# Kernel optimization log

Hardware: AMD Instinct MI355X
Metric: run time of the kernel (lower is better)

## Reference

```python
import jax, jax.numpy as jnp
import numpy as np

LATENT = 64
COND = 768
HEADS = 8
R = 8           # LoRA rank
SCALING = 1.0   # lora_alpha / r
SCALE = (LATENT / HEADS) ** -0.5


def _lora_linear(x, W, b, A, B):
    # loralib-style: y = x W^T + b + scaling * (x A^T) B^T
    return x @ W.T + b + SCALING * ((x @ A.T) @ B.T)


def setup_inputs() -> dict:
    key = jax.random.key(0)
    ks = jax.random.split(key, 20)
    B, C, H, W_ = 16, LATENT, 64, 64
    L = 77
    z = jax.random.normal(ks[0], (B, C, H, W_), dtype=jnp.float32)
    cond = jax.random.normal(ks[1], (B, L, COND), dtype=jnp.float32)

    def lin(k, out_d, in_d):
        k1, k2, k3 = jax.random.split(k, 3)
        W = jax.random.normal(k1, (out_d, in_d), dtype=jnp.float32) * 0.02
        b = jnp.zeros((out_d,), dtype=jnp.float32)
        A = jax.random.normal(k2, (R, in_d), dtype=jnp.float32) * 0.02
        Bm = jax.random.normal(k3, (out_d, R), dtype=jnp.float32) * 0.02
        return W, b, A, Bm

    Wq, bq, Aq, Bq = lin(ks[2], LATENT, LATENT)
    Wk, bk, Ak, Bk = lin(ks[3], LATENT, COND)
    Wv, bv, Av, Bv = lin(ks[4], LATENT, COND)
    Wo, bo, Ao, Bo = lin(ks[5], LATENT, LATENT)
    return dict(z=z, cond=cond,
                Wq=Wq, bq=bq, Aq=Aq, Bq=Bq,
                Wk=Wk, bk=bk, Ak=Ak, Bk=Bk,
                Wv=Wv, bv=bv, Av=Av, Bv=Bv,
                Wo=Wo, bo=bo, Ao=Ao, Bo=Bo)


def reference(z, cond, Wq, bq, Aq, Bq, Wk, bk, Ak, Bk, Wv, bv, Av, Bv, Wo, bo, Ao, Bo):
    B, C, H, W_ = z.shape
    hw = H * W_
    dh = C // HEADS
    z_flat = z.transpose(0, 2, 3, 1).reshape(B, hw, C)  # [B, hw, C]

    q = _lora_linear(z_flat, Wq, bq, Aq, Bq)   # [B, hw, C]
    k = _lora_linear(cond, Wk, bk, Ak, Bk)     # [B, L, C]
    v = _lora_linear(cond, Wv, bv, Av, Bv)     # [B, L, C]

    q = q.reshape(B, hw, HEADS, dh).transpose(0, 2, 1, 3)  # [B, h, hw, dh]
    k = k.reshape(B, -1, HEADS, dh).transpose(0, 2, 1, 3)  # [B, h, L, dh]
    v = v.reshape(B, -1, HEADS, dh).transpose(0, 2, 1, 3)

    dots = jnp.einsum('bhqd,bhkd->bhqk', q, k) * SCALE  # [B, h, hw, L]
    attn = jax.nn.softmax(dots, axis=-1)
    out = jnp.einsum('bhqk,bhkd->bhqd', attn, v)        # [B, h, hw, dh]
    out = out.transpose(0, 2, 1, 3).reshape(B, hw, C)
    out = _lora_linear(out, Wo, bo, Ao, Bo)
    return out.reshape(B, H, W_, C).transpose(0, 3, 1, 2)  # [B, C, H, W]
```

## Files before the change

kernel.cpp:

```cpp
#include <hip/hip_runtime.h>


#define HW   4096
#define CHN  64
#define LSEQ 77
#define CD   768
#define NB   16

#define OFF_WQ 0
#define OFF_WK 4096
#define OFF_WV 53248
#define OFF_WO 102400
#define OFF_K  106496
#define OFF_V  185344

#define QF 0.51011784563163f

__global__ __launch_bounds__(256) void prep_weights(
    const float* __restrict__ Wq, const float* __restrict__ Aq, const float* __restrict__ Bq,
    const float* __restrict__ Wk, const float* __restrict__ Ak, const float* __restrict__ Bk,
    const float* __restrict__ Wv, const float* __restrict__ Av, const float* __restrict__ Bv,
    const float* __restrict__ Wo, const float* __restrict__ Ao, const float* __restrict__ Bo,
    float* __restrict__ ws) {
  int idx = blockIdx.x * 256 + threadIdx.x;
  const float *W, *A, *Bm;
  float* out;
  int in_d, local;
  float scale = 1.0f;
  if (idx < 4096)        { W = Wq; A = Aq; Bm = Bq; out = ws + OFF_WQ; in_d = 64;  local = idx; scale = QF; }
  else if (idx < 53248)  { W = Wk; A = Ak; Bm = Bk; out = ws + OFF_WK; in_d = 768; local = idx - 4096; }
  else if (idx < 102400) { W = Wv; A = Av; Bm = Bv; out = ws + OFF_WV; in_d = 768; local = idx - 53248; }
  else                   { W = Wo; A = Ao; Bm = Bo; out = ws + OFF_WO; in_d = 64;  local = idx - 102400; }
  int co = local & 63;
  int c  = local >> 6;
  float val = W[co * in_d + c];
  #pragma unroll
  for (int r = 0; r < 8; r++) val += Bm[co * 8 + r] * A[r * in_d + c];
  out[local] = val * scale;
}

__global__ __launch_bounds__(256) void kvproj5(
    const float* __restrict__ cond,
    const float* __restrict__ wkT,
    const float* __restrict__ wvT,
    const float* __restrict__ bk, const float* __restrict__ bv,
    float* __restrict__ kbuf,
    float* __restrict__ vbuf) {
  __shared__ float xs[4 * CD];
  __shared__ float red[16 * 256];
  int kv = blockIdx.y;
  int r0 = blockIdx.x * 4;
  int t  = threadIdx.x;
  int l  = t & 63;
  int q  = __builtin_amdgcn_readfirstlane(t >> 6);
  int l16 = l & 15;
  int cs  = l >> 4;

  {
    const float4* src = (const float4*)(cond + r0 * CD);
    float4* dst = (float4*)xs;
    #pragma unroll
    for (int i = 0; i < 3; i++) dst[t + 256 * i] = src[t + 256 * i];
  }
  __syncthreads();

  const float4* wT4 = (const float4*)(kv ? wvT : wkT);
  float4 a0 = make_float4(0.f, 0.f, 0.f, 0.f);
  float4 a1 = a0, a2 = a0, a3 = a0;
  int cbase = q * 192 + cs;
  #pragma unroll 8
  for (int it = 0; it < 48; it++) {
    int c = cbase + 4 * it;
    float4 w  = wT4[c * 16 + l16];
    float x0 = xs[0 * CD + c];
    float x1 = xs[1 * CD + c];
    float x2 = xs[2 * CD + c];
    float x3 = xs[3 * CD + c];
    a0.x = fmaf(x0, w.x, a0.x); a0.y = fmaf(x0, w.y, a0.y);
    a0.z = fmaf(x0, w.z, a0.z); a0.w = fmaf(x0, w.w, a0.w);
    a1.x = fmaf(x1, w.x, a1.x); a1.y = fmaf(x1, w.y, a1.y);
    a1.z = fmaf(x1, w.z, a1.z); a1.w = fmaf(x1, w.w, a1.w);
    a2.x = fmaf(x2, w.x, a2.x); a2.y = fmaf(x2, w.y, a2.y);
    a2.z = fmaf(x2, w.z, a2.z); a2.w = fmaf(x2, w.w, a2.w);
    a3.x = fmaf(x3, w.x, a3.x); a3.y = fmaf(x3, w.y, a3.y);
    a3.z = fmaf(x3, w.z, a3.z); a3.w = fmaf(x3, w.w, a3.w);
  }

  {
    float4* redq = (float4*)(red + (q * 4 + cs) * 256);
    redq[0 * 16 + l16] = a0;
    redq[1 * 16 + l16] = a1;
    redq[2 * 16 + l16] = a2;
    redq[3 * 16 + l16] = a3;
  }
  __syncthreads();

  int r  = t >> 6;
  int co = t & 63;
  float val = (kv ? bv : bk)[co];
  #pragma unroll
  for (int g = 0; g < 16; g++) val += red[g * 256 + r * 64 + co];
  (kv ? vbuf : kbuf)[(r0 + r) * 64 + co] = val;
}

__global__ __launch_bounds__(256, 2) void megattn(
    const float* __restrict__ z,
    const float* __restrict__ wqT,
    const float* __restrict__ bq,
    const float* __restrict__ kbuf,
    const float* __restrict__ vbuf,
    const float* __restrict__ woT,
    const float* __restrict__ bo,
    float* __restrict__ out) {
  __shared__ float smem[LSEQ * 64 * 2];
  int b  = blockIdx.y;
  int p0 = blockIdx.x * 128;
  int t  = threadIdx.x;
  int h  = t >> 5;
  int pl = t & 31;

  float* ks = smem;
  float* vs = smem + LSEQ * 64;
  {
    const float4* ksrc = (const float4*)(kbuf + b * LSEQ * 64);
    const float4* vsrc = (const float4*)(vbuf + b * LSEQ * 64);
    float4* kd = (float4*)ks;
    float4* vd = (float4*)vs;
    for (int i = t; i < LSEQ * 16; i += 256) { kd[i] = ksrc[i]; vd[i] = vsrc[i]; }
  }

  float qr[4][8];
  {
    const float4 b0 = *(const float4*)(bq + 8 * h);
    const float4 b1 = *(const float4*)(bq + 8 * h + 4);
    #pragma unroll
    for (int i = 0; i < 4; i++) {
      qr[i][0] = b0.x * QF; qr[i][1] = b0.y * QF; qr[i][2] = b0.z * QF; qr[i][3] = b0.w * QF;
      qr[i][4] = b1.x * QF; qr[i][5] = b1.y * QF; qr[i][6] = b1.z * QF; qr[i][7] = b1.w * QF;
    }
  }
  const float* zb = z + b * (CHN * HW) + p0 + pl;
  #pragma unroll 4
  for (int c = 0; c < 64; c++) {
    float4 w0 = *(const float4*)(wqT + c * 64 + 8 * h);
    float4 w1 = *(const float4*)(wqT + c * 64 + 8 * h + 4);
    float zv[4];
    #pragma unroll
    for (int i = 0; i < 4; i++) zv[i] = zb[c * HW + 32 * i];
    #pragma unroll
    for (int i = 0; i < 4; i++) {
      qr[i][0] = fmaf(zv[i], w0.x, qr[i][0]);
      qr[i][1] = fmaf(zv[i], w0.y, qr[i][1]);
      qr[i][2] = fmaf(zv[i], w0.z, qr[i][2]);
      qr[i][3] = fmaf(zv[i], w0.w, qr[i][3]);
      qr[i][4] = fmaf(zv[i], w1.x, qr[i][4]);
      qr[i][5] = fmaf(zv[i], w1.y, qr[i][5]);
      qr[i][6] = fmaf(zv[i], w1.z, qr[i][6]);
      qr[i][7] = fmaf(zv[i], w1.w, qr[i][7]);
    }
  }
  __syncthreads();

  float acc[4][8];
  float li[4];
  #pragma unroll
  for (int i = 0; i < 4; i++) {
    li[i] = 0.f;
    #pragma unroll
    for (int d = 0; d < 8; d++) acc[i][d] = 0.f;
  }
  #pragma unroll 2
  for (int j = 0; j < LSEQ; j++) {
    float4 k0 = *(const float4*)(ks + j * 64 + 8 * h);
    float4 k1 = *(const float4*)(ks + j * 64 + 8 * h + 4);
    float4 v0 = *(const float4*)(vs + j * 64 + 8 * h);
    float4 v1 = *(const float4*)(vs + j * 64 + 8 * h + 4);
    #pragma unroll
    for (int i = 0; i < 4; i++) {
      float s = qr[i][0] * k0.x;
      s = fmaf(qr[i][1], k0.y, s);
      s = fmaf(qr[i][2], k0.z, s);
      s = fmaf(qr[i][3], k0.w, s);
      s = fmaf(qr[i][4], k1.x, s);
      s = fmaf(qr[i][5], k1.y, s);
      s = fmaf(qr[i][6], k1.z, s);
      s = fmaf(qr[i][7], k1.w, s);
      float e = __builtin_amdgcn_exp2f(s);
      li[i] += e;
      acc[i][0] = fmaf(e, v0.x, acc[i][0]);
      acc[i][1] = fmaf(e, v0.y, acc[i][1]);
      acc[i][2] = fmaf(e, v0.z, acc[i][2]);
      acc[i][3] = fmaf(e, v0.w, acc[i][3]);
      acc[i][4] = fmaf(e, v1.x, acc[i][4]);
      acc[i][5] = fmaf(e, v1.y, acc[i][5]);
      acc[i][6] = fmaf(e, v1.z, acc[i][6]);
      acc[i][7] = fmaf(e, v1.w, acc[i][7]);
    }
  }
  __syncthreads();

  float* ao = smem;
  #pragma unroll
  for (int i = 0; i < 4; i++) {
    float inv = 1.0f / li[i];
    int p = pl + 32 * i;
    #pragma unroll
    for (int d = 0; d < 8; d++) ao[p * 65 + 8 * h + d] = acc[i][d] * inv;
  }
  __syncthreads();

  int q2 = t & 127;
  int chalf = __builtin_amdgcn_readfirstlane((t >> 7) & 1);
  float acc2[32];
  #pragma unroll
  for (int j2 = 0; j2 < 32; j2++) acc2[j2] = bo[chalf * 32 + j2];
  const float* aor = ao + q2 * 65;
  #pragma unroll 4
  for (int c = 0; c < 64; c++) {
    float xv = aor[c];
    const float* wr = woT + c * 64 + chalf * 32;
    #pragma unroll
    for (int j2 = 0; j2 < 32; j2++) acc2[j2] = fmaf(xv, wr[j2], acc2[j2]);
  }
  float* ob = out + b * (CHN * HW) + p0 + q2;
  #pragma unroll
  for (int j2 = 0; j2 < 32; j2++) ob[(chalf * 32 + j2) * HW] = acc2[j2];
}

extern "C" void kernel_launch(void* const* d_in, const int* in_sizes, int n_in,
                              void* d_out, int out_size, void* d_ws, size_t ws_size,
                              hipStream_t stream) {
  const float* z    = (const float*)d_in[0];
  const float* cond = (const float*)d_in[1];
  const float* Wq = (const float*)d_in[2];  const float* bq = (const float*)d_in[3];
  const float* Aq = (const float*)d_in[4];  const float* Bq = (const float*)d_in[5];
  const float* Wk = (const float*)d_in[6];  const float* bk = (const float*)d_in[7];
  const float* Ak = (const float*)d_in[8];  const float* Bk = (const float*)d_in[9];
  const float* Wv = (const float*)d_in[10]; const float* bv = (const float*)d_in[11];
  const float* Av = (const float*)d_in[12]; const float* Bv = (const float*)d_in[13];
  const float* Wo = (const float*)d_in[14]; const float* bo = (const float*)d_in[15];
  const float* Ao = (const float*)d_in[16]; const float* Bo = (const float*)d_in[17];
  float* ws  = (float*)d_ws;
  float* out = (float*)d_out;

  prep_weights<<<416, 256, 0, stream>>>(Wq, Aq, Bq, Wk, Ak, Bk, Wv, Av, Bv, Wo, Ao, Bo, ws);
  kvproj5<<<dim3(308, 2), 256, 0, stream>>>(cond, ws + OFF_WK, ws + OFF_WV, bk, bv,
                                            ws + OFF_K, ws + OFF_V);
  megattn<<<dim3(32, 16), 256, 0, stream>>>(z, ws + OFF_WQ, bq, ws + OFF_K, ws + OFF_V,
                                            ws + OFF_WO, bo, out);
}
```

Before: 148.1 us.

## Fuse LoRA weight prep into K/V projection kernel, applying LoRA as low-rank update

Result: slower. 158.3 us (+6.9%).

```diff
diff --git a/kernel.cpp b/kernel.cpp
--- a/kernel.cpp
+++ b/kernel.cpp
@@ -8,51 +8,29 @@
 #define NB   16
 
 #define OFF_WQ 0
-#define OFF_WK 4096
-#define OFF_WV 53248
 #define OFF_WO 102400
 #define OFF_K  106496
 #define OFF_V  185344
 
 #define QF 0.51011784563163f
 
-__global__ __launch_bounds__(256) void prep_weights(
-    const float* __restrict__ Wq, const float* __restrict__ Aq, const float* __restrict__ Bq,
+__global__ __launch_bounds__(256) void kvproj6(
+    const float* __restrict__ cond,
     const float* __restrict__ Wk, const float* __restrict__ Ak, const float* __restrict__ Bk,
     const float* __restrict__ Wv, const float* __restrict__ Av, const float* __restrict__ Bv,
+    const float* __restrict__ bk, const float* __restrict__ bv,
+    const float* __restrict__ Wq, const float* __restrict__ Aq, const float* __restrict__ Bq,
     const float* __restrict__ Wo, const float* __restrict__ Ao, const float* __restrict__ Bo,
     float* __restrict__ ws) {
-  int idx = blockIdx.x * 256 + threadIdx.x;
-  const float *W, *A, *Bm;
-  float* out;
-  int in_d, local;
-  float scale = 1.0f;
-  if (idx < 4096)        { W = Wq; A = Aq; Bm = Bq; out = ws + OFF_WQ; in_d = 64;  local = idx; scale = QF; }
-  else if (idx < 53248)  { W = Wk; A = Ak; Bm = Bk; out = ws + OFF_WK; in_d = 768; local = idx - 4096; }
-  else if (idx < 102400) { W = Wv; A = Av; Bm = Bv; out = ws + OFF_WV; in_d = 768; local = idx - 53248; }
-  else                   { W = Wo; A = Ao; Bm = Bo; out = ws + OFF_WO; in_d = 64;  local = idx - 102400; }
-  int co = local & 63;
-  int c  = local >> 6;
-  float val = W[co * in_d + c];
-  #pragma unroll
-  for (int r = 0; r < 8; r++) val += Bm[co * 8 + r] * A[r * in_d + c];
-  out[local] = val * scale;
-}
-
-__global__ __launch_bounds__(256) void kvproj5(
-    const float* __restrict__ cond,
-    const float* __restrict__ wkT,
-    const float* __restrict__ wvT,
-    const float* __restrict__ bk, const float* __restrict__ bv,
-    float* __restrict__ kbuf,
-    float* __restrict__ vbuf) {
   __shared__ float xs[4 * CD];
+  __shared__ float wlds[64 * 65];
   __shared__ float red[16 * 256];
+  __shared__ float axs[4 * 8];
   int kv = blockIdx.y;
   int r0 = blockIdx.x * 4;
   int t  = threadIdx.x;
   int l  = t & 63;
-  int q  = __builtin_amdgcn_readfirstlane(t >> 6);
+  int w  = __builtin_amdgcn_readfirstlane(t >> 6);
   int l16 = l & 15;
   int cs  = l >> 4;
 
@@ -64,30 +42,59 @@
   }
   __syncthreads();
 
-  const float4* wT4 = (const float4*)(kv ? wvT : wkT);
+  {
+    int rr = (t >> 3) & 7;
+    int oct = t & 7;
+    const float* Arow = (kv ? Av : Ak) + rr * CD;
+    const float* xrow = xs + w * CD;
+    float part = 0.f;
+    #pragma unroll 8
+    for (int i = 0; i < 96; i++) part = fmaf(Arow[oct + 8 * i], xrow[oct + 8 * i], part);
+    part += __shfl_xor(part, 1);
+    part += __shfl_xor(part, 2);
+    part += __shfl_xor(part, 4);
+    if (oct == 0) axs[w * 8 + rr] = part;
+  }
+
+  const float* Wsrc = kv ? Wv : Wk;
   float4 a0 = make_float4(0.f, 0.f, 0.f, 0.f);
   float4 a1 = a0, a2 = a0, a3 = a0;
-  int cbase = q * 192 + cs;
-  #pragma unroll 8
-  for (int it = 0; it < 48; it++) {
-    int c = cbase + 4 * it;
-    float4 w  = wT4[c * 16 + l16];
-    float x0 = xs[0 * CD + c];
-    float x1 = xs[1 * CD + c];
-    float x2 = xs[2 * CD + c];
-    float x3 = xs[3 * CD + c];
-    a0.x = fmaf(x0, w.x, a0.x); a0.y = fmaf(x0, w.y, a0.y);
-    a0.z = fmaf(x0, w.z, a0.z); a0.w = fmaf(x0, w.w, a0.w);
-    a1.x = fmaf(x1, w.x, a1.x); a1.y = fmaf(x1, w.y, a1.y);
-    a1.z = fmaf(x1, w.z, a1.z); a1.w = fmaf(x1, w.w, a1.w);
-    a2.x = fmaf(x2, w.x, a2.x); a2.y = fmaf(x2, w.y, a2.y);
-    a2.z = fmaf(x2, w.z, a2.z); a2.w = fmaf(x2, w.w, a2.w);
-    a3.x = fmaf(x3, w.x, a3.x); a3.y = fmaf(x3, w.y, a3.y);
-    a3.z = fmaf(x3, w.z, a3.z); a3.w = fmaf(x3, w.w, a3.w);
-  }
-
-  {
-    float4* redq = (float4*)(red + (q * 4 + cs) * 256);
+  int co_s = t >> 2, q4 = t & 3;
+  for (int ch = 0; ch < 12; ch++) {
+    __syncthreads();
+    {
+      const float* wp = Wsrc + co_s * CD + ch * 64 + q4 * 16;
+      #pragma unroll
+      for (int i = 0; i < 4; i++) {
+        float4 wv4 = *(const float4*)(wp + 4 * i);
+        wlds[(q4 * 16 + 4 * i + 0) * 65 + co_s] = wv4.x;
+        wlds[(q4 * 16 + 4 * i + 1) * 65 + co_s] = wv4.y;
+        wlds[(q4 * 16 + 4 * i + 2) * 65 + co_s] = wv4.z;
+        wlds[(q4 * 16 + 4 * i + 3) * 65 + co_s] = wv4.w;
+      }
+    }
+    __syncthreads();
+    #pragma unroll
+    for (int it = 0; it < 4; it++) {
+      int c  = w * 16 + cs + 4 * it;
+      int gc = ch * 64 + c;
+      float4 wv = *(const float4*)(wlds + c * 65 + l16 * 4);
+      float x0 = xs[0 * CD + gc];
+      float x1 = xs[1 * CD + gc];
+      float x2 = xs[2 * CD + gc];
+      float x3 = xs[3 * CD + gc];
+      a0.x = fmaf(x0, wv.x, a0.x); a0.y = fmaf(x0, wv.y, a0.y);
+      a0.z = fmaf(x0, wv.z, a0.z); a0.w = fmaf(x0, wv.w, a0.w);
+      a1.x = fmaf(x1, wv.x, a1.x); a1.y = fmaf(x1, wv.y, a1.y);
+      a1.z = fmaf(x1, wv.z, a1.z); a1.w = fmaf(x1, wv.w, a1.w);
+      a2.x = fmaf(x2, wv.x, a2.x); a2.y = fmaf(x2, wv.y, a2.y);
+      a2.z = fmaf(x2, wv.z, a2.z); a2.w = fmaf(x2, wv.w, a2.w);
+      a3.x = fmaf(x3, wv.x, a3.x); a3.y = fmaf(x3, wv.y, a3.y);
+      a3.z = fmaf(x3, wv.z, a3.z); a3.w = fmaf(x3, wv.w, a3.w);
+    }
+  }
+  {
+    float4* redq = (float4*)(red + (w * 4 + cs) * 256);
     redq[0 * 16 + l16] = a0;
     redq[1 * 16 + l16] = a1;
     redq[2 * 16 + l16] = a2;
@@ -95,12 +102,33 @@
   }
   __syncthreads();
 
-  int r  = t >> 6;
-  int co = t & 63;
-  float val = (kv ? bv : bk)[co];
-  #pragma unroll
-  for (int g = 0; g < 16; g++) val += red[g * 256 + r * 64 + co];
-  (kv ? vbuf : kbuf)[(r0 + r) * 64 + co] = val;
+  {
+    int r  = t >> 6;
+    int co = t & 63;
+    float val = (kv ? bv : bk)[co];
+    #pragma unroll
+    for (int g = 0; g < 16; g++) val += red[g * 256 + r * 64 + co];
+    const float* Bm = kv ? Bv : Bk;
+    #pragma unroll
+    for (int j = 0; j < 8; j++) val = fmaf(Bm[co * 8 + j], axs[r * 8 + j], val);
+    (ws + (kv ? OFF_V : OFF_K))[(r0 + r) * 64 + co] = val;
+  }
+
+  if (kv == 0 && blockIdx.x < 32) {
+    int idx = blockIdx.x * 256 + t;
+    const float *W, *A, *Bm;
+    float* o;
+    float scale;
+    int local;
+    if (idx < 4096) { W = Wq; A = Aq; Bm = Bq; o = ws + OFF_WQ; local = idx;        scale = QF;   }
+    else            { W = Wo; A = Ao; Bm = Bo; o = ws + OFF_WO; local = idx - 4096; scale = 1.0f; }
+    int co = local & 63;
+    int c  = local >> 6;
+    float val = W[co * 64 + c];
+    #pragma unroll
+    for (int r = 0; r < 8; r++) val += Bm[co * 8 + r] * A[r * 64 + c];
+    o[local] = val * scale;
+  }
 }
 
 __global__ __launch_bounds__(256, 2) void megattn(
@@ -243,9 +271,8 @@
   float* ws  = (float*)d_ws;
   float* out = (float*)d_out;
 
-  prep_weights<<<416, 256, 0, stream>>>(Wq, Aq, Bq, Wk, Ak, Bk, Wv, Av, Bv, Wo, Ao, Bo, ws);
-  kvproj5<<<dim3(308, 2), 256, 0, stream>>>(cond, ws + OFF_WK, ws + OFF_WV, bk, bv,
-                                            ws + OFF_K, ws + OFF_V);
+  kvproj6<<<dim3(308, 2), 256, 0, stream>>>(cond, Wk, Ak, Bk, Wv, Av, Bv, bk, bv,
+                                            Wq, Aq, Bq, Wo, Ao, Bo, ws);
   megattn<<<dim3(32, 16), 256, 0, stream>>>(z, ws + OFF_WQ, bq, ws + OFF_K, ws + OFF_V,
                                             ws + OFF_WO, bo, out);
 }
```
